# Kernel optimization log

Hardware: AMD Instinct MI355X
Metric: run time of the kernel (lower is better)

## Reference

```python
import jax, jax.numpy as jnp
import numpy as np

NEG_POS_RATIO = 3

def hard_negative_mining(bg_loss, labels, neg_pos_ratio):
    # bg_loss: [B, P] = -log_softmax(conf)[..., 0]; labels: [B, P] int
    pos_mask = labels > 0                               # [B, P]
    num_pos = jnp.sum(pos_mask, axis=1, keepdims=True)  # [B, 1]
    num_neg = num_pos * neg_pos_ratio                   # [B, 1]
    # positives are excluded from the negative ranking
    masked = jnp.where(pos_mask, -jnp.inf, bg_loss)
    # rank of each prior when sorted by loss descending (0 = hardest negative)
    order = jnp.argsort(jnp.argsort(-masked, axis=1), axis=1)
    neg_mask = order < num_neg
    return pos_mask | neg_mask

def setup_inputs() -> dict:
    key = jax.random.key(0)
    k1, k2, k3, k4, k5 = jax.random.split(key, 5)
    B, P, C = 64, 8732, 81
    pred_loc = jax.random.normal(k1, (B, P, 4), dtype=jnp.float32)
    pred_conf = jax.random.normal(k2, (B, P, C), dtype=jnp.float32)
    gt_loc = jax.random.normal(k3, (B, P, 4), dtype=jnp.float32)
    raw_labels = jax.random.randint(k4, (B, P), 0, C)
    is_pos = jax.random.uniform(k5, (B, P)) < 0.02
    gt_labels = jnp.where(is_pos, raw_labels, 0).astype(jnp.int32)
    return {"pred_loc": pred_loc, "pred_conf": pred_conf, "gt_loc": gt_loc, "gt_labels": gt_labels}

def reference(pred_loc, pred_conf, gt_loc, gt_labels):
    # SSD MultiBox loss (training-mode forward of MultiBoxHeads)
    logp = jax.nn.log_softmax(pred_conf, axis=-1)           # [B, P, C]
    bg_loss = -logp[..., 0]                                 # [B, P]
    mask = jax.lax.stop_gradient(
        hard_negative_mining(jax.lax.stop_gradient(bg_loss), gt_labels, NEG_POS_RATIO))
    # cross-entropy with gt labels, summed over kept (pos + hard-neg) priors
    ce = -jnp.take_along_axis(logp, gt_labels[..., None].astype(jnp.int32), axis=-1)[..., 0]
    objectness_loss = jnp.sum(jnp.where(mask, ce, 0.0))
    # smooth L1 on positive priors only
    pos_mask = gt_labels > 0                                # [B, P]
    diff = pred_loc - gt_loc
    absd = jnp.abs(diff)
    sl1 = jnp.where(absd < 1.0, 0.5 * diff * diff, absd - 0.5)
    smooth_l1_loss = jnp.sum(jnp.where(pos_mask[..., None], sl1, 0.0))
    num_pos = jnp.maximum(jnp.sum(pos_mask), 1).astype(jnp.float32)
    return (objectness_loss / num_pos, smooth_l1_loss / num_pos)
```

## Files before the change

kernel.cpp:

```cpp
#include <hip/hip_runtime.h>
#include <cstdint>
#include <cstddef>

#define BATCH 64
#define PRI   8732
#define NCLS  81
#define NEGPOS 3
#define NTOT  (BATCH * PRI)
#define PPB   64
#define NWIN  (NTOT / PPB)
#define WFLOATS (PPB * NCLS)
#define WF4   (WFLOATS / 4)
#define NPERS 768

__device__ __forceinline__ unsigned keymap(float f) {
    unsigned u = __float_as_uint(f);
    return (u & 0x80000000u) ? ~u : (u | 0x80000000u);
}

__device__ __forceinline__ void gl_lds16(const float4* g, float4* l) {
    __builtin_amdgcn_global_load_lds(
        (const __attribute__((address_space(1))) void*)(const void*)g,
        (__attribute__((address_space(3))) void*)(void*)l, 16, 0, 0);
}

__global__ __launch_bounds__(256) void k_lse(const float* __restrict__ conf,
                                             const int* __restrict__ labels,
                                             const float* __restrict__ ploc,
                                             const float* __restrict__ gloc,
                                             unsigned* __restrict__ keysg,
                                             float* __restrict__ cepart,
                                             float* __restrict__ slpart) {
    __shared__ float lds[2][WFLOATS];
    __shared__ int   labs[2][PPB];
    __shared__ float red0[4], red1[4];
    const int t = threadIdx.x;
    const int bid = blockIdx.x;

    float ceacc = 0.0f, slacc = 0.0f;

    auto stage = [&](int buf, int w) {
        const float4* g4 = reinterpret_cast<const float4*>(conf) + (size_t)w * WF4;
        float4* l4 = reinterpret_cast<float4*>(&lds[buf][0]);
#pragma unroll
        for (int j = 0; j < 5; ++j) gl_lds16(&g4[t + 256 * j], &l4[t + 256 * j]);
        if (t < WF4 - 1280) gl_lds16(&g4[t + 1280], &l4[t + 1280]);
        if (t < PPB) labs[buf][t] = labels[w * PPB + t];
    };

    stage(0, bid);
    __syncthreads();

    int cur = 0;
    for (int i = 0; ; ++i) {
        const int w  = bid + i * NPERS;
        const int wn = w + NPERS;
        const bool more = (wn < NWIN);
        if (more) stage(cur ^ 1, wn);

        const float* ldsw = &lds[cur][0];
        const int q   = t >> 2, h = t & 3;
        const int f0  = q * NCLS + 20 * h;
        const int len = (h == 3) ? 21 : 20;
        const int a0  = f0 & ~3;
        const int o   = f0 & 3;
        const int ve  = o + len;

        const float4* lp = reinterpret_cast<const float4*>(ldsw + a0);
        float4 v0 = lp[0], v1 = lp[1], v2 = lp[2], v3 = lp[3], v4 = lp[4], v5 = lp[5];
        v0.x = (o > 0) ? -INFINITY : v0.x;
        v0.y = (o > 1) ? -INFINITY : v0.y;
        v0.z = (o > 2) ? -INFINITY : v0.z;
        v5.x = (ve > 20) ? v5.x : -INFINITY;
        v5.y = (ve > 21) ? v5.y : -INFINITY;
        v5.z = (ve > 22) ? v5.z : -INFINITY;
        v5.w = (ve > 23) ? v5.w : -INFINITY;

        float m;
        {
            float a = fmaxf(fmaxf(v0.x, v0.y), fmaxf(v0.z, v0.w));
            float c = fmaxf(fmaxf(v1.x, v1.y), fmaxf(v1.z, v1.w));
            float d = fmaxf(fmaxf(v2.x, v2.y), fmaxf(v2.z, v2.w));
            float e = fmaxf(fmaxf(v3.x, v3.y), fmaxf(v3.z, v3.w));
            float f = fmaxf(fmaxf(v4.x, v4.y), fmaxf(v4.z, v4.w));
            float g = fmaxf(fmaxf(v5.x, v5.y), fmaxf(v5.z, v5.w));
            m = fmaxf(fmaxf(fmaxf(a, c), fmaxf(d, e)), fmaxf(f, g));
        }
        float s =
            __expf(v0.x - m) + __expf(v0.y - m) + __expf(v0.z - m) + __expf(v0.w - m) +
            __expf(v1.x - m) + __expf(v1.y - m) + __expf(v1.z - m) + __expf(v1.w - m) +
            __expf(v2.x - m) + __expf(v2.y - m) + __expf(v2.z - m) + __expf(v2.w - m) +
            __expf(v3.x - m) + __expf(v3.y - m) + __expf(v3.z - m) + __expf(v3.w - m) +
            __expf(v4.x - m) + __expf(v4.y - m) + __expf(v4.z - m) + __expf(v4.w - m) +
            __expf(v5.x - m) + __expf(v5.y - m) + __expf(v5.z - m) + __expf(v5.w - m);

#pragma unroll
        for (int off = 1; off <= 2; off <<= 1) {
            const float mo = __shfl_xor(m, off, 64);
            const float so = __shfl_xor(s, off, 64);
            const float mn = fmaxf(m, mo);
            s = s * __expf(m - mn) + so * __expf(mo - mn);
            m = mn;
        }
        const float lse = m + __logf(s);

        if (h == 0) {
            const int p   = w * PPB + q;
            const int lab = labs[cur][q];
            const float c0 = ldsw[q * NCLS];
            unsigned key = 0u;
            if (lab > 0) {
                ceacc += lse - ldsw[q * NCLS + lab];
                const float4 pl = *reinterpret_cast<const float4*>(ploc + (size_t)p * 4);
                const float4 gl = *reinterpret_cast<const float4*>(gloc + (size_t)p * 4);
                float d, a;
                d = pl.x - gl.x; a = fabsf(d); slacc += (a < 1.0f) ? 0.5f * d * d : a - 0.5f;
                d = pl.y - gl.y; a = fabsf(d); slacc += (a < 1.0f) ? 0.5f * d * d : a - 0.5f;
                d = pl.z - gl.z; a = fabsf(d); slacc += (a < 1.0f) ? 0.5f * d * d : a - 0.5f;
                d = pl.w - gl.w; a = fabsf(d); slacc += (a < 1.0f) ? 0.5f * d * d : a - 0.5f;
            } else {
                key = keymap(lse - c0);
            }
            keysg[p] = key;
        }

        if (!more) break;
        __syncthreads();
        cur ^= 1;
    }

#pragma unroll
    for (int off = 32; off > 0; off >>= 1) {
        ceacc += __shfl_xor(ceacc, off, 64);
        slacc += __shfl_xor(slacc, off, 64);
    }
    const int wid = t >> 6, lane = t & 63;
    __syncthreads();
    if (lane == 0) { red0[wid] = ceacc; red1[wid] = slacc; }
    __syncthreads();
    if (t == 0) {
        cepart[bid] = red0[0] + red0[1] + red0[2] + red0[3];
        slpart[bid] = red1[0] + red1[1] + red1[2] + red1[3];
    }
}

__global__ __launch_bounds__(1024) void k_row(const unsigned* __restrict__ keysg,
                                              float* __restrict__ rowobj,
                                              float* __restrict__ rownp) {
    __shared__ unsigned keys_s[PRI];
    __shared__ unsigned hist[16][257];
    __shared__ unsigned ured[16];
    __shared__ float    fred[16];
    __shared__ unsigned sh_prefix, sh_r;
    __shared__ int      sh_flag;

    const int row  = blockIdx.x;
    const int tid  = threadIdx.x;
    const int wid  = tid >> 6;
    const int lane = tid & 63;
    const unsigned* krow = keysg + (size_t)row * PRI;

    unsigned np = 0;
    for (int j = tid; j < PRI; j += 1024) {
        const unsigned key = krow[j];
        keys_s[j] = key;
        np += (key == 0u) ? 1u : 0u;
    }
#pragma unroll
    for (int off = 32; off > 0; off >>= 1) np += __shfl_xor(np, off, 64);
    if (lane == 0) ured[wid] = np;
    __syncthreads();
    unsigned num_pos = 0;
#pragma unroll
    for (int w = 0; w < 16; ++w) num_pos += ured[w];
    const int k = (int)num_pos * NEGPOS;

    unsigned Kstar = 0xFFFFFFFFu;
    int r_eq = 0;
    bool take_all = false;
    if (k > 0) {
        unsigned prefix = 0;
        int r = k, flag = 0;
        unsigned* hist_flat = &hist[0][0];
        for (int level = 3; level >= 0; --level) {
            const int shift = level * 8;
            for (int i = tid; i < 16 * 257; i += 1024) hist_flat[i] = 0;
            __syncthreads();
            for (int j = tid; j < PRI; j += 1024) {
                const unsigned key = keys_s[j];
                if (key == 0u) continue;
                if (level < 3 && (key >> (shift + 8)) != (prefix >> (shift + 8))) continue;
                atomicAdd(&hist[wid][(key >> shift) & 255u], 1u);
            }
            __syncthreads();
            if (wid == 0) {
                const int b0 = lane * 4;
                unsigned h0 = 0, h1 = 0, h2 = 0, h3 = 0;
#pragma unroll
                for (int w = 0; w < 16; ++w) {
                    h0 += hist[w][b0]; h1 += hist[w][b0 + 1];
                    h2 += hist[w][b0 + 2]; h3 += hist[w][b0 + 3];
                }
                const unsigned loc = h0 + h1 + h2 + h3;
                unsigned ssum = loc;
#pragma unroll
                for (int o2 = 1; o2 < 64; o2 <<= 1) {
                    const unsigned t2 = __shfl_down(ssum, o2, 64);
                    if (lane + o2 < 64) ssum += t2;
                }
                const unsigned above = ssum - loc;
                const unsigned cum3 = above + h3;
                const unsigned cum2 = cum3 + h2;
                const unsigned cum1 = cum2 + h1;
                const unsigned cum0 = cum1 + h0;
                const unsigned long long msk = __ballot(cum0 >= (unsigned)r);
                if (msk == 0ULL) {
                    if (lane == 0) sh_flag = 1;
                } else {
                    const int L = 63 - __clzll(msk);
                    if (lane == L) {
                        unsigned selbin, cumsel, hsel;
                        if      (cum3 >= (unsigned)r) { selbin = b0 + 3; cumsel = cum3; hsel = h3; }
                        else if (cum2 >= (unsigned)r) { selbin = b0 + 2; cumsel = cum2; hsel = h2; }
                        else if (cum1 >= (unsigned)r) { selbin = b0 + 1; cumsel = cum1; hsel = h1; }
                        else                          { selbin = b0;     cumsel = cum0; hsel = h0; }
                        sh_prefix = prefix | (selbin << shift);
                        sh_r = (unsigned)r - (cumsel - hsel);
                        sh_flag = 0;
                    }
                }
            }
            __syncthreads();
            flag = sh_flag;
            if (flag) break;
            prefix = sh_prefix;
            r = (int)sh_r;
        }
        take_all = (flag != 0);
        if (!take_all) { Kstar = prefix; r_eq = r; }
    }

    float obj = 0.0f;
    if (k > 0) {
        for (int j = tid; j < PRI; j += 1024) {
            const unsigned key = keys_s[j];
            if (key != 0u && (take_all || key > Kstar))
                obj += __uint_as_float(key ^ 0x80000000u);
        }
        if (tid == 0 && !take_all)
            obj += (float)r_eq * __uint_as_float(Kstar ^ 0x80000000u);
    }

#pragma unroll
    for (int off = 32; off > 0; off >>= 1) obj += __shfl_xor(obj, off, 64);
    __syncthreads();
    if (lane == 0) fred[wid] = obj;
    __syncthreads();
    if (tid == 0) {
        float to = 0.0f;
#pragma unroll
        for (int w = 0; w < 16; ++w) to += fred[w];
        rowobj[row] = to;
        rownp[row]  = (float)num_pos;
    }
}

__global__ __launch_bounds__(256) void k_final(const float* __restrict__ cepart,
                                               const float* __restrict__ slpart,
                                               const float* __restrict__ rowobj,
                                               const float* __restrict__ rownp,
                                               float* __restrict__ out) {
    const int tid = threadIdx.x;
    float ce = 0.0f, sl = 0.0f;
    for (int i = tid; i < NPERS; i += 256) { ce += cepart[i]; sl += slpart[i]; }
    float ro = 0.0f, np = 0.0f;
    if (tid < BATCH) { ro = rowobj[tid]; np = rownp[tid]; }
#pragma unroll
    for (int off = 32; off > 0; off >>= 1) {
        ce += __shfl_xor(ce, off, 64);
        sl += __shfl_xor(sl, off, 64);
        ro += __shfl_xor(ro, off, 64);
        np += __shfl_xor(np, off, 64);
    }
    __shared__ float r0[4], r1[4], r2[4], r3[4];
    const int wid = tid >> 6, lane = tid & 63;
    if (lane == 0) { r0[wid] = ce; r1[wid] = sl; r2[wid] = ro; r3[wid] = np; }
    __syncthreads();
    if (tid == 0) {
        const float tce = r0[0] + r0[1] + r0[2] + r0[3];
        const float tsl = r1[0] + r1[1] + r1[2] + r1[3];
        const float tro = r2[0] + r2[1] + r2[2] + r2[3];
        const float tnp = r3[0] + r3[1] + r3[2] + r3[3];
        const float npos = fmaxf(tnp, 1.0f);
        out[0] = (tce + tro) / npos;
        out[1] = tsl / npos;
    }
}

extern "C" void kernel_launch(void* const* d_in, const int* in_sizes, int n_in,
                              void* d_out, int out_size, void* d_ws, size_t ws_size,
                              hipStream_t stream) {
    const float* pred_loc  = (const float*)d_in[0];
    const float* pred_conf = (const float*)d_in[1];
    const float* gt_loc    = (const float*)d_in[2];
    const int*   gt_labels = (const int*)d_in[3];
    float* out = (float*)d_out;

    unsigned* keysg   = (unsigned*)d_ws;
    float*    cepart  = (float*)(keysg + NTOT);
    float*    slpart  = cepart + NPERS;
    float*    rowobj  = slpart + NPERS;
    float*    rownp   = rowobj + BATCH;

    k_lse<<<NPERS, 256, 0, stream>>>(pred_conf, gt_labels, pred_loc, gt_loc,
                                     keysg, cepart, slpart);
    k_row<<<BATCH, 1024, 0, stream>>>(keysg, rowobj, rownp);
    k_final<<<1, 256, 0, stream>>>(cepart, slpart, rowobj, rownp, out);
}
```

Before: 57.38 us.

## Fuse final reduction into row kernel and build top-level histogram during load

Removes the separate final-reduction kernel by having the last row block, chosen with an atomic ticket counter, perform the global reduction, which saves one launch. The first radix level's histogram is now built while keys are loaded, using wave-aggregated atomics on a single shared histogram instead of 16 per-wave copies, so one pass over shared memory is skipped. A memset of the counter is added to each call, and the later histogram levels now contend on a single shared copy.

```diff
diff --git a/kernel.cpp b/kernel.cpp
--- a/kernel.cpp
+++ b/kernel.cpp
@@ -145,12 +145,16 @@
 }
 
 __global__ __launch_bounds__(1024) void k_row(const unsigned* __restrict__ keysg,
+                                              const float* __restrict__ cepart,
+                                              const float* __restrict__ slpart,
+                                              unsigned* __restrict__ counter,
                                               float* __restrict__ rowobj,
-                                              float* __restrict__ rownp) {
+                                              float* __restrict__ rownp,
+                                              float* __restrict__ out) {
     __shared__ unsigned keys_s[PRI];
-    __shared__ unsigned hist[16][257];
+    __shared__ unsigned hist[256];
     __shared__ unsigned ured[16];
-    __shared__ float    fred[16];
+    __shared__ float    fred[16], fred2[16];
     __shared__ unsigned sh_prefix, sh_r;
     __shared__ int      sh_flag;
 
@@ -160,11 +164,28 @@
     const int lane = tid & 63;
     const unsigned* krow = keysg + (size_t)row * PRI;
 
+    if (tid < 256) hist[tid] = 0;
+    __syncthreads();
+
     unsigned np = 0;
-    for (int j = tid; j < PRI; j += 1024) {
-        const unsigned key = krow[j];
-        keys_s[j] = key;
-        np += (key == 0u) ? 1u : 0u;
+    for (int jb = 0; jb < PRI; jb += 1024) {
+        const int j = jb + tid;
+        const bool in = (j < PRI);
+        const unsigned key = in ? krow[j] : 0u;
+        if (in) keys_s[j] = key;
+        np += (in && key == 0u) ? 1u : 0u;
+        bool act = in && (key != 0u);
+        const unsigned bin = key >> 24;
+        while (true) {
+            const unsigned long long msk = __ballot(act);
+            if (msk == 0ULL) break;
+            const int leader = __ffsll(msk) - 1;
+            const unsigned lbin = __shfl(bin, leader, 64);
+            const bool same = act && (bin == lbin);
+            const unsigned cnt = (unsigned)__popcll(__ballot(same));
+            if (lane == leader) atomicAdd(&hist[lbin], cnt);
+            act = act && !same;
+        }
     }
 #pragma unroll
     for (int off = 32; off > 0; off >>= 1) np += __shfl_xor(np, off, 64);
@@ -181,26 +202,23 @@
     if (k > 0) {
         unsigned prefix = 0;
         int r = k, flag = 0;
-        unsigned* hist_flat = &hist[0][0];
         for (int level = 3; level >= 0; --level) {
             const int shift = level * 8;
-            for (int i = tid; i < 16 * 257; i += 1024) hist_flat[i] = 0;
-            __syncthreads();
-            for (int j = tid; j < PRI; j += 1024) {
-                const unsigned key = keys_s[j];
-                if (key == 0u) continue;
-                if (level < 3 && (key >> (shift + 8)) != (prefix >> (shift + 8))) continue;
-                atomicAdd(&hist[wid][(key >> shift) & 255u], 1u);
+            if (level < 3) {
+                if (tid < 256) hist[tid] = 0;
+                __syncthreads();
+                for (int j = tid; j < PRI; j += 1024) {
+                    const unsigned key = keys_s[j];
+                    if (key == 0u) continue;
+                    if ((key >> (shift + 8)) != (prefix >> (shift + 8))) continue;
+                    atomicAdd(&hist[(key >> shift) & 255u], 1u);
+                }
+                __syncthreads();
             }
-            __syncthreads();
             if (wid == 0) {
                 const int b0 = lane * 4;
-                unsigned h0 = 0, h1 = 0, h2 = 0, h3 = 0;
-#pragma unroll
-                for (int w = 0; w < 16; ++w) {
-                    h0 += hist[w][b0]; h1 += hist[w][b0 + 1];
-                    h2 += hist[w][b0 + 2]; h3 += hist[w][b0 + 3];
-                }
+                const unsigned h0 = hist[b0], h1 = hist[b0 + 1];
+                const unsigned h2 = hist[b0 + 2], h3 = hist[b0 + 3];
                 const unsigned loc = h0 + h1 + h2 + h3;
                 unsigned ssum = loc;
 #pragma unroll
@@ -262,38 +280,36 @@
         for (int w = 0; w < 16; ++w) to += fred[w];
         rowobj[row] = to;
         rownp[row]  = (float)num_pos;
-    }
-}
-
-__global__ __launch_bounds__(256) void k_final(const float* __restrict__ cepart,
-                                               const float* __restrict__ slpart,
-                                               const float* __restrict__ rowobj,
-                                               const float* __restrict__ rownp,
-                                               float* __restrict__ out) {
-    const int tid = threadIdx.x;
-    float ce = 0.0f, sl = 0.0f;
-    for (int i = tid; i < NPERS; i += 256) { ce += cepart[i]; sl += slpart[i]; }
-    float ro = 0.0f, np = 0.0f;
-    if (tid < BATCH) { ro = rowobj[tid]; np = rownp[tid]; }
-#pragma unroll
-    for (int off = 32; off > 0; off >>= 1) {
-        ce += __shfl_xor(ce, off, 64);
-        sl += __shfl_xor(sl, off, 64);
-        ro += __shfl_xor(ro, off, 64);
-        np += __shfl_xor(np, off, 64);
-    }
-    __shared__ float r0[4], r1[4], r2[4], r3[4];
-    const int wid = tid >> 6, lane = tid & 63;
-    if (lane == 0) { r0[wid] = ce; r1[wid] = sl; r2[wid] = ro; r3[wid] = np; }
-    __syncthreads();
-    if (tid == 0) {
-        const float tce = r0[0] + r0[1] + r0[2] + r0[3];
-        const float tsl = r1[0] + r1[1] + r1[2] + r1[3];
-        const float tro = r2[0] + r2[1] + r2[2] + r2[3];
-        const float tnp = r3[0] + r3[1] + r3[2] + r3[3];
-        const float npos = fmaxf(tnp, 1.0f);
-        out[0] = (tce + tro) / npos;
-        out[1] = tsl / npos;
+        __threadfence();
+        const unsigned ticket = atomicAdd(counter, 1u);
+        sh_flag = (ticket == BATCH - 1) ? -1 : 0;
+    }
+    __syncthreads();
+    if (sh_flag == -1) {
+        __threadfence();
+        float ce = 0.0f, sl = 0.0f, ro = 0.0f, np2 = 0.0f;
+        if (tid < NPERS) { ce = cepart[tid]; sl = slpart[tid]; }
+        if (tid < BATCH) { ro = rowobj[tid]; np2 = rownp[tid]; }
+#pragma unroll
+        for (int off = 32; off > 0; off >>= 1) {
+            ce  += __shfl_xor(ce,  off, 64);
+            sl  += __shfl_xor(sl,  off, 64);
+            ro  += __shfl_xor(ro,  off, 64);
+            np2 += __shfl_xor(np2, off, 64);
+        }
+        __syncthreads();
+        if (lane == 0) { fred[wid] = ce + ro; fred2[wid] = sl; ured[wid] = __float_as_uint(np2); }
+        __syncthreads();
+        if (tid == 0) {
+            float tobj = 0.0f, tsl = 0.0f, tnp = 0.0f;
+#pragma unroll
+            for (int w = 0; w < 16; ++w) {
+                tobj += fred[w]; tsl += fred2[w]; tnp += __uint_as_float(ured[w]);
+            }
+            const float npos = fmaxf(tnp, 1.0f);
+            out[0] = tobj / npos;
+            out[1] = tsl / npos;
+        }
     }
 }
 
@@ -306,14 +322,16 @@
     const int*   gt_labels = (const int*)d_in[3];
     float* out = (float*)d_out;
 
-    unsigned* keysg   = (unsigned*)d_ws;
+    unsigned* counter = (unsigned*)d_ws;
+    unsigned* keysg   = (unsigned*)d_ws + 4;
     float*    cepart  = (float*)(keysg + NTOT);
     float*    slpart  = cepart + NPERS;
     float*    rowobj  = slpart + NPERS;
     float*    rownp   = rowobj + BATCH;
 
+    hipMemsetAsync(counter, 0, 16, stream);
     k_lse<<<NPERS, 256, 0, stream>>>(pred_conf, gt_labels, pred_loc, gt_loc,
                                      keysg, cepart, slpart);
-    k_row<<<BATCH, 1024, 0, stream>>>(keysg, rowobj, rownp);
-    k_final<<<1, 256, 0, stream>>>(cepart, slpart, rowobj, rownp, out);
-}
+    k_row<<<BATCH, 1024, 0, stream>>>(keysg, cepart, slpart, counter,
+                                      rowobj, rownp, out);
+}
```

Measured after the change: 59.42 us. 1.04x slower.

## Replace async global-to-LDS double buffer with register-staged single LDS buffer

Applied to the files above, without the earlier changes.

Replaces the direct global_load_lds double-buffered staging with a register prefetch: the next window is loaded into VGPRs while the current window is processed, then written to a single LDS buffer between two barriers. This halves LDS use, which may allow more blocks per CU, and replaces the async LDS DMA path with ordinary loads. In exchange it uses more registers, adds a second barrier per iteration, and serialises the LDS write with compute.

```diff
diff --git a/kernel.cpp b/kernel.cpp
--- a/kernel.cpp
+++ b/kernel.cpp
@@ -18,12 +18,6 @@
     return (u & 0x80000000u) ? ~u : (u | 0x80000000u);
 }
 
-__device__ __forceinline__ void gl_lds16(const float4* g, float4* l) {
-    __builtin_amdgcn_global_load_lds(
-        (const __attribute__((address_space(1))) void*)(const void*)g,
-        (__attribute__((address_space(3))) void*)(void*)l, 16, 0, 0);
-}
-
 __global__ __launch_bounds__(256) void k_lse(const float* __restrict__ conf,
                                              const int* __restrict__ labels,
                                              const float* __restrict__ ploc,
@@ -31,34 +25,49 @@
                                              unsigned* __restrict__ keysg,
                                              float* __restrict__ cepart,
                                              float* __restrict__ slpart) {
-    __shared__ float lds[2][WFLOATS];
-    __shared__ int   labs[2][PPB];
+    __shared__ float lds[WFLOATS];
+    __shared__ int   labs[PPB];
     __shared__ float red0[4], red1[4];
     const int t = threadIdx.x;
     const int bid = blockIdx.x;
 
     float ceacc = 0.0f, slacc = 0.0f;
 
-    auto stage = [&](int buf, int w) {
-        const float4* g4 = reinterpret_cast<const float4*>(conf) + (size_t)w * WF4;
-        float4* l4 = reinterpret_cast<float4*>(&lds[buf][0]);
-#pragma unroll
-        for (int j = 0; j < 5; ++j) gl_lds16(&g4[t + 256 * j], &l4[t + 256 * j]);
-        if (t < WF4 - 1280) gl_lds16(&g4[t + 1280], &l4[t + 1280]);
-        if (t < PPB) labs[buf][t] = labels[w * PPB + t];
+    const float4* conf4 = reinterpret_cast<const float4*>(conf);
+    float4 r0 = {0,0,0,0}, r1 = r0, r2 = r0, r3 = r0, r4 = r0, r5 = r0;
+    int labr = 0;
+
+    auto loadreg = [&](int w) {
+        const float4* g4 = conf4 + (size_t)w * WF4;
+        r0 = g4[t];
+        r1 = g4[t + 256];
+        r2 = g4[t + 512];
+        r3 = g4[t + 768];
+        r4 = g4[t + 1024];
+        if (t < WF4 - 1280) r5 = g4[t + 1280];
+        if (t < PPB) labr = labels[w * PPB + t];
     };
-
-    stage(0, bid);
-    __syncthreads();
-
-    int cur = 0;
+    auto writelds = [&]() {
+        float4* l4 = reinterpret_cast<float4*>(lds);
+        l4[t]        = r0;
+        l4[t + 256]  = r1;
+        l4[t + 512]  = r2;
+        l4[t + 768]  = r3;
+        l4[t + 1024] = r4;
+        if (t < WF4 - 1280) l4[t + 1280] = r5;
+        if (t < PPB) labs[t] = labr;
+    };
+
+    loadreg(bid);
+    writelds();
+    if (bid + NPERS < NWIN) loadreg(bid + NPERS);
+    __syncthreads();
+
     for (int i = 0; ; ++i) {
         const int w  = bid + i * NPERS;
         const int wn = w + NPERS;
         const bool more = (wn < NWIN);
-        if (more) stage(cur ^ 1, wn);
-
-        const float* ldsw = &lds[cur][0];
+
         const int q   = t >> 2, h = t & 3;
         const int f0  = q * NCLS + 20 * h;
         const int len = (h == 3) ? 21 : 20;
@@ -66,7 +75,7 @@
         const int o   = f0 & 3;
         const int ve  = o + len;
 
-        const float4* lp = reinterpret_cast<const float4*>(ldsw + a0);
+        const float4* lp = reinterpret_cast<const float4*>(lds + a0);
         float4 v0 = lp[0], v1 = lp[1], v2 = lp[2], v3 = lp[3], v4 = lp[4], v5 = lp[5];
         v0.x = (o > 0) ? -INFINITY : v0.x;
         v0.y = (o > 1) ? -INFINITY : v0.y;
@@ -106,11 +115,11 @@
 
         if (h == 0) {
             const int p   = w * PPB + q;
-            const int lab = labs[cur][q];
-            const float c0 = ldsw[q * NCLS];
+            const int lab = labs[q];
+            const float c0 = lds[q * NCLS];
             unsigned key = 0u;
             if (lab > 0) {
-                ceacc += lse - ldsw[q * NCLS + lab];
+                ceacc += lse - lds[q * NCLS + lab];
                 const float4 pl = *reinterpret_cast<const float4*>(ploc + (size_t)p * 4);
                 const float4 gl = *reinterpret_cast<const float4*>(gloc + (size_t)p * 4);
                 float d, a;
@@ -126,7 +135,9 @@
 
         if (!more) break;
         __syncthreads();
-        cur ^= 1;
+        writelds();
+        if (wn + NPERS < NWIN) loadreg(wn + NPERS);
+        __syncthreads();
     }
 
 #pragma unroll
```

After: 56.81 us. No clear change (-1.0%).
